# Kernel tuning notes

Hardware: AMD Instinct MI355X
Metric: run time of the kernel (lower is better)

## Reference

```python
import jax, jax.numpy as jnp
import numpy as np

B, T_MAX, U_MAX, V = 8, 256, 128, 512
NULL_INDEX = 0


def setup_inputs() -> dict:
    key = jax.random.key(0)
    k1, k2, k3, k4 = jax.random.split(key, 4)
    logits = jax.random.normal(k1, (B, T_MAX, U_MAX + 1, V), dtype=jnp.float32)
    y = jax.random.randint(k2, (B, U_MAX), 1, V, dtype=jnp.int32)  # non-blank labels
    T_len = jax.random.randint(k3, (B,), T_MAX // 2, T_MAX + 1, dtype=jnp.int32)
    U_len = jax.random.randint(k4, (B,), U_MAX // 2, U_MAX + 1, dtype=jnp.int32)
    return {"logits": logits, "y": y, "T_len": T_len, "U_len": U_len}


def _rnnt_loss(logits, y, T_len, T_len_unused=None, U_len=None):
    raise NotImplementedError


def reference(logits, y, T_len, U_len):
    # logits: (B, T, U+1, V) raw joiner output; apply log_softmax as in compute_loss
    logp = jax.nn.log_softmax(logits, axis=-1)
    Bn = logits.shape[0]
    blank = logp[..., NULL_INDEX]                                   # (B, T, U+1)
    # emit[b, t, u] = logp[b, t, u, y[b, u]] for u in [0, U_max)
    emit = jnp.take_along_axis(
        logp[:, :, :-1, :], y[:, None, :, None], axis=3)[..., 0]    # (B, T, U)
    # ce[b, t, u] = sum_{k<u} emit[b, t, k] (cumulative emission log-prob)
    ce_all = jnp.concatenate(
        [jnp.zeros((Bn, logits.shape[1], 1), logp.dtype),
         jnp.cumsum(emit, axis=2)], axis=2)                          # (B, T, U+1)

    # Row t=0: alpha[0, u] = sum_{k<u} emit[0, k]
    row0 = ce_all[:, 0, :]                                           # (B, U+1)

    # Row recursion (vectorized over u via log-domain prefix trick):
    # alpha[t, u] = logsumexp_{u'<=u}( a[u'] + ce[t, u] - ce[t, u'] ),
    # with a[u'] = alpha[t-1, u'] + blank[t-1, u'].
    def step(row_prev, xs):
        blank_prev, ce_t = xs                # each (B, U+1)
        a = row_prev + blank_prev
        row = ce_t + jax.lax.associative_scan(jnp.logaddexp, a - ce_t, axis=1)
        return row, row

    xs = (jnp.moveaxis(blank[:, :-1, :], 0, 1),   # (T-1, B, U+1)
          jnp.moveaxis(ce_all[:, 1:, :], 0, 1))   # (T-1, B, U+1)
    _, rows = jax.lax.scan(step, row0, xs)
    alpha = jnp.moveaxis(jnp.concatenate([row0[None], rows], axis=0), 0, 1)  # (B, T, U+1)

    bidx = jnp.arange(Bn)
    log_probs = alpha[bidx, T_len - 1, U_len] + blank[bidx, T_len - 1, U_len]
    return -jnp.mean(log_probs)
```

## Files before the change

### kernel.cpp

```cpp
#include <hip/hip_runtime.h>

#define BN   8
#define TMAX 256
#define UMAX 128
#define U1   129
#define VV   512
#define SD   392

__device__ __forceinline__ float logaddexpf_(float a, float b) {
    float mx = fmaxf(a, b);
    float d  = fabsf(a - b);
    return mx + log1pf(__expf(-d));
}

__global__ __launch_bounds__(256) void lse_extract(
        const float* __restrict__ logits,
        const int*   __restrict__ y,
        const int*   __restrict__ Tl,
        const int*   __restrict__ Ul,
        float* __restrict__ blankD,
        float* __restrict__ emitD) {
    int lane = threadIdx.x & 63;
    int row  = blockIdx.x * 4 + (threadIdx.x >> 6);
    if (row >= BN * TMAX * U1) return;
    int b   = row / (TMAX * U1);
    int rem = row - b * (TMAX * U1);
    int t   = rem / U1;
    int u   = rem - t * U1;
    if (t >= Tl[b] || u > Ul[b]) return;

    const float4* base = (const float4*)(logits + (size_t)row * VV);
    float4 r0 = base[lane * 2];
    float4 r1 = base[lane * 2 + 1];

    float m = fmaxf(fmaxf(fmaxf(r0.x, r0.y), fmaxf(r0.z, r0.w)),
                    fmaxf(fmaxf(r1.x, r1.y), fmaxf(r1.z, r1.w)));
#pragma unroll
    for (int off = 32; off > 0; off >>= 1) m = fmaxf(m, __shfl_xor(m, off));

    float s = __expf(r0.x - m) + __expf(r0.y - m) + __expf(r0.z - m) + __expf(r0.w - m)
            + __expf(r1.x - m) + __expf(r1.y - m) + __expf(r1.z - m) + __expf(r1.w - m);
#pragma unroll
    for (int off = 32; off > 0; off >>= 1) s += __shfl_xor(s, off);

    float lse = m + __logf(s);
    int sd = t + u;
    if (lane == 0)
        blankD[((size_t)b * SD + sd) * U1 + u] = r0.x - lse;
    if (u < UMAX) {
        int yv = y[b * UMAX + u];
        if ((yv >> 3) == lane) {
            int e = yv & 7;
            float v = (e == 0) ? r0.x : (e == 1) ? r0.y : (e == 2) ? r0.z : (e == 3) ? r0.w
                    : (e == 4) ? r1.x : (e == 5) ? r1.y : (e == 6) ? r1.z : r1.w;
            emitD[((size_t)b * SD + sd) * UMAX + u] = v - lse;
        }
    }
}

__global__ __launch_bounds__(192) void dp_wavefront(
        const float* __restrict__ blankD,
        const float* __restrict__ emitD,
        const int*   __restrict__ Tlp,
        const int*   __restrict__ Ulp,
        float* __restrict__ out) {
    __shared__ float buf[2][U1 + 4];
    int b = blockIdx.x;
    int u = threadIdx.x;
    int Tl = Tlp[b], Ul = Ulp[b];
    int dend = Tl - 1 + Ul;
    const float* bD = blankD + (size_t)b * SD * U1;
    const float* eD = emitD  + (size_t)b * SD * UMAX;
    bool act_u = (u < U1);
    int  ue    = (u == 0) ? 0 : u - 1;

    float pb[2], pe[2];
    if (act_u) {
        pb[1] = bD[(size_t)0 * U1   + u];
        pe[1] = eD[(size_t)0 * UMAX + ue];
        pb[0] = bD[(size_t)1 * U1   + u];
        pe[0] = eD[(size_t)1 * UMAX + ue];
    }
    if (u == 0) buf[0][0] = 0.0f;
    __syncthreads();

    for (int d = 1; d <= dend; ++d) {
        int par = d & 1;
        int ulo = d - (Tl - 1); if (ulo < 0) ulo = 0;
        int uhi = (d < Ul) ? d : Ul;
        if (act_u && u >= ulo && u <= uhi) {
            float cur;
            if (u == 0) {
                cur = buf[par ^ 1][0] + pb[par];
            } else if (u == d) {
                cur = buf[par ^ 1][u - 1] + pe[par];
            } else {
                float up = buf[par ^ 1][u]     + pb[par];
                float lf = buf[par ^ 1][u - 1] + pe[par];
                cur = logaddexpf_(up, lf);
            }
            buf[par][u] = cur;
            if (d == dend && u == Ul) {
                float lp = cur + bD[(size_t)dend * U1 + Ul];
                atomicAdd(out, -lp * (1.0f / BN));
            }
        }
        if (act_u) {
            pb[par] = bD[(size_t)(d + 1) * U1   + u];
            pe[par] = eD[(size_t)(d + 1) * UMAX + ue];
        }
        __syncthreads();
    }
}

extern "C" void kernel_launch(void* const* d_in, const int* in_sizes, int n_in,
                              void* d_out, int out_size, void* d_ws, size_t ws_size,
                              hipStream_t stream) {
    const float* logits = (const float*)d_in[0];
    const int*   y      = (const int*)d_in[1];
    const int*   Tl     = (const int*)d_in[2];
    const int*   Ul     = (const int*)d_in[3];
    float* out = (float*)d_out;

    float* blankD = (float*)d_ws;
    float* emitD  = blankD + (size_t)BN * SD * U1;

    hipMemsetAsync(d_out, 0, sizeof(float), stream);

    int rows = BN * TMAX * U1;
    lse_extract<<<dim3((rows + 3) / 4), dim3(256), 0, stream>>>(
        logits, y, Tl, Ul, blankD, emitD);
    dp_wavefront<<<dim3(BN), dim3(192), 0, stream>>>(blankD, emitD, Tl, Ul, out);
}
```

Baseline: 870.8 us.

## Run DP wavefront per wavefront with shuffles and register prefetch, drop barriers

```diff
diff --git a/kernel.cpp b/kernel.cpp
--- a/kernel.cpp
+++ b/kernel.cpp
@@ -6,11 +6,14 @@
 #define U1   129
 #define VV   512
 #define SD   392
+#define PS   132
+#define NEG  -1e30f
+#define PF   4
 
 __device__ __forceinline__ float logaddexpf_(float a, float b) {
     float mx = fmaxf(a, b);
     float d  = fabsf(a - b);
-    return mx + log1pf(__expf(-d));
+    return mx + __logf(1.0f + __expf(-d));
 }
 
 __global__ __launch_bounds__(256) void lse_extract(
@@ -46,70 +49,88 @@
     float lse = m + __logf(s);
     int sd = t + u;
     if (lane == 0)
-        blankD[((size_t)b * SD + sd) * U1 + u] = r0.x - lse;
+        blankD[((size_t)b * SD + sd) * PS + u] = r0.x - lse;
     if (u < UMAX) {
         int yv = y[b * UMAX + u];
         if ((yv >> 3) == lane) {
             int e = yv & 7;
             float v = (e == 0) ? r0.x : (e == 1) ? r0.y : (e == 2) ? r0.z : (e == 3) ? r0.w
                     : (e == 4) ? r1.x : (e == 5) ? r1.y : (e == 6) ? r1.z : r1.w;
-            emitD[((size_t)b * SD + sd) * UMAX + u] = v - lse;
+            emitD[((size_t)b * SD + sd) * PS + (u + 1)] = v - lse;
         }
     }
 }
 
-__global__ __launch_bounds__(192) void dp_wavefront(
+__global__ __launch_bounds__(512) void dp_fused(
         const float* __restrict__ blankD,
         const float* __restrict__ emitD,
         const int*   __restrict__ Tlp,
         const int*   __restrict__ Ulp,
         float* __restrict__ out) {
-    __shared__ float buf[2][U1 + 4];
-    int b = blockIdx.x;
-    int u = threadIdx.x;
-    int Tl = Tlp[b], Ul = Ulp[b];
+    __shared__ float part[BN];
+    int w = threadIdx.x >> 6;
+    int L = threadIdx.x & 63;
+    int Tl = Tlp[w], Ul = Ulp[w];
     int dend = Tl - 1 + Ul;
-    const float* bD = blankD + (size_t)b * SD * U1;
-    const float* eD = emitD  + (size_t)b * SD * UMAX;
-    bool act_u = (u < U1);
-    int  ue    = (u == 0) ? 0 : u - 1;
+    const float* bD = blankD + (size_t)w * SD * PS;
+    const float* eD = emitD  + (size_t)w * SD * PS;
 
-    float pb[2], pe[2];
-    if (act_u) {
-        pb[1] = bD[(size_t)0 * U1   + u];
-        pe[1] = eD[(size_t)0 * UMAX + ue];
-        pb[0] = bD[(size_t)1 * U1   + u];
-        pe[0] = eD[(size_t)1 * UMAX + ue];
+    int  u0 = 2 * L, u1 = 2 * L + 1;
+    bool lx = (L == 63);
+
+    float p0 = (L == 0) ? 0.0f : NEG;
+    float p1 = NEG, px = NEG;
+
+    float rb0[PF], rb1[PF], re0[PF], re1[PF], rbx[PF], rex[PF];
+#pragma unroll
+    for (int i = 0; i < PF; ++i) {
+        float2 fb = *(const float2*)(bD + i * PS + u0);
+        float2 fe = *(const float2*)(eD + i * PS + u0);
+        rb0[i] = fb.x; rb1[i] = fb.y; re0[i] = fe.x; re1[i] = fe.y;
+        rbx[i] = lx ? bD[i * PS + 128] : NEG;
+        rex[i] = lx ? eD[i * PS + 128] : NEG;
     }
-    if (u == 0) buf[0][0] = 0.0f;
-    __syncthreads();
 
     for (int d = 1; d <= dend; ++d) {
-        int par = d & 1;
+        int r = (d - 1) & (PF - 1);
+        float b0 = rb0[r], b1 = rb1[r], e0 = re0[r], e1 = re1[r];
+        float bx = rbx[r], ex = rex[r];
+
+        float pm1 = __shfl_up(p1, 1);
+        if (L == 0) pm1 = NEG;
+
         int ulo = d - (Tl - 1); if (ulo < 0) ulo = 0;
         int uhi = (d < Ul) ? d : Ul;
-        if (act_u && u >= ulo && u <= uhi) {
-            float cur;
-            if (u == 0) {
-                cur = buf[par ^ 1][0] + pb[par];
-            } else if (u == d) {
-                cur = buf[par ^ 1][u - 1] + pe[par];
-            } else {
-                float up = buf[par ^ 1][u]     + pb[par];
-                float lf = buf[par ^ 1][u - 1] + pe[par];
-                cur = logaddexpf_(up, lf);
-            }
-            buf[par][u] = cur;
-            if (d == dend && u == Ul) {
-                float lp = cur + bD[(size_t)dend * U1 + Ul];
-                atomicAdd(out, -lp * (1.0f / BN));
-            }
-        }
-        if (act_u) {
-            pb[par] = bD[(size_t)(d + 1) * U1   + u];
-            pe[par] = eD[(size_t)(d + 1) * UMAX + ue];
-        }
-        __syncthreads();
+
+        float c0 = logaddexpf_(p0 + b0, pm1 + e0);
+        float c1 = logaddexpf_(p1 + b1, p0  + e1);
+        float cx = logaddexpf_(px + bx, p1  + ex);
+
+        p0 = (u0 >= ulo && u0 <= uhi) ? c0 : NEG;
+        p1 = (u1 >= ulo && u1 <= uhi) ? c1 : NEG;
+        px = (lx && 128 >= ulo && 128 <= uhi) ? cx : NEG;
+
+        int s = d - 1 + PF;
+        float2 fb = *(const float2*)(bD + s * PS + u0);
+        float2 fe = *(const float2*)(eD + s * PS + u0);
+        rb0[r] = fb.x; rb1[r] = fb.y; re0[r] = fe.x; re1[r] = fe.y;
+        if (lx) { rbx[r] = bD[s * PS + 128]; rex[r] = eD[s * PS + 128]; }
+    }
+
+    bool own;
+    float afin;
+    if (Ul == 128) { own = lx; afin = px; }
+    else           { own = (L == (Ul >> 1)); afin = (Ul & 1) ? p1 : p0; }
+    if (own) {
+        float lp = afin + bD[(size_t)dend * PS + Ul];
+        part[w] = lp;
+    }
+    __syncthreads();
+    if (threadIdx.x == 0) {
+        float acc = 0.0f;
+#pragma unroll
+        for (int i = 0; i < BN; ++i) acc += part[i];
+        *out = -acc * (1.0f / BN);
     }
 }
 
@@ -123,12 +144,10 @@
     float* out = (float*)d_out;
 
     float* blankD = (float*)d_ws;
-    float* emitD  = blankD + (size_t)BN * SD * U1;
-
-    hipMemsetAsync(d_out, 0, sizeof(float), stream);
+    float* emitD  = blankD + (size_t)BN * SD * PS;
 
     int rows = BN * TMAX * U1;
     lse_extract<<<dim3((rows + 3) / 4), dim3(256), 0, stream>>>(
         logits, y, Tl, Ul, blankD, emitD);
-    dp_wavefront<<<dim3(BN), dim3(192), 0, stream>>>(blankD, emitD, Tl, Ul, out);
+    dp_fused<<<dim3(1), dim3(BN * 64), 0, stream>>>(blankD, emitD, Tl, Ul, out);
 }
```

After: 891.3 us. +2.4%, slower.
